# Optimization experiments

Hardware: AMD Instinct MI355X
Metric: run time of the kernel (lower is better)

The kernel has to match this reference:

```python
import jax, jax.numpy as jnp
import numpy as np

E = 65536          # number of edges (cell pairs)
D = 256            # hidden_dim
P = 8              # n_lr_pairs


def setup_inputs() -> dict:
    key = jax.random.key(0)
    k1, k2, k3, k4, k5, k6, k7 = jax.random.split(key, 7)
    scale = 1.0 / np.sqrt(D)
    z_src = jax.random.normal(k1, (E, D), dtype=jnp.float32)
    z_dst = jax.random.normal(k2, (E, D), dtype=jnp.float32)
    lr_pair_idx = jax.random.randint(k3, (E,), 0, P, dtype=jnp.int64)
    # Per-LR-pair Linear(D, D): y = x @ W.T + b  (torch convention, W: [out, in])
    W_lr = jax.random.normal(k4, (P, D, D), dtype=jnp.float32) * scale
    b_lr = jax.random.normal(k5, (P, D), dtype=jnp.float32) * scale
    # nn.Bilinear(D, D, 1): weight [1, D, D], bias [1]
    W_bil = jax.random.normal(k6, (1, D, D), dtype=jnp.float32) * scale
    b_bil = jax.random.normal(k7, (1,), dtype=jnp.float32) * scale
    return {"z_src": z_src, "z_dst": z_dst, "W_lr": W_lr, "b_lr": b_lr,
            "W_bil": W_bil, "b_bil": b_bil, "lr_pair_idx": lr_pair_idx}


def _forward(z_src, z_dst, W_lr, b_lr, W_bil, b_bil, lr_pair_idx):
    # Per-LR-pair linear projection of z_src (MoE-style routing).
    # Fixed small loop over P experts; each iteration is a dense GEMM over
    # all E edges, masked to the edges routed to that pair. All idx values
    # lie in [0, P), so the zeros-init in the original is fully overwritten.
    z_proj = jnp.zeros_like(z_src)
    for p in range(P):
        mask = (lr_pair_idx == p)[:, None]                      # [E, 1]
        y_p = z_src @ W_lr[p].T + b_lr[p]                       # [E, D]
        z_proj = jnp.where(mask, y_p, z_proj)
    # Bilinear scoring: score_e = z_proj_e @ W_bil[0] @ z_dst_e + b_bil
    t = z_proj @ W_bil[0]                                       # [E, D]
    scores = jnp.sum(t * z_dst, axis=-1, keepdims=True) + b_bil  # [E, 1]
    return scores


def reference(z_src, z_dst, W_lr, b_lr, W_bil, b_bil, lr_pair_idx):
    return _forward(z_src, z_dst, W_lr, b_lr, W_bil, b_bil, lr_pair_idx)
```

## Files before the change

### kernel.cpp

```cpp
#include <hip/hip_runtime.h>
#include <hip/hip_bf16.h>
#include <cstddef>

#define NE 65536
#define ND 256
#define NP 8
#define CAP 16384
#define TMAX 256
#define RBLK 64
#define EPB (NE / RBLK)

typedef short bf16x8 __attribute__((ext_vector_type(8)));
typedef float f32x4  __attribute__((ext_vector_type(4)));

__device__ __forceinline__ unsigned short f2bf(float f) {
  unsigned int u = __float_as_uint(f);
  u += 0x7FFFu + ((u >> 16) & 1u);
  return (unsigned short)(u >> 16);
}

__device__ __forceinline__ int sniff_is32(const void* idxraw, int* lflag) {
  int tid = threadIdx.x;
  if (tid == 0) *lflag = 0;
  __syncthreads();
  const unsigned int* w = (const unsigned int*)idxraw;
  unsigned int val = w[(blockIdx.x * 256 + tid) * 2 + 1];
  if (__any(val != 0) && (tid & 63) == 0) atomicOr(lflag, 1);
  __syncthreads();
  return *lflag;
}

__device__ __forceinline__ int load_idx(const void* idxraw, int is32, int e) {
  return is32 ? ((const int*)idxraw)[e] : (int)((const long long*)idxraw)[e];
}

__global__ __launch_bounds__(256) void k_hist(const void* __restrict__ idxraw,
                                              int* __restrict__ counts) {
  __shared__ int h[NP];
  __shared__ int lflag;
  int tid = threadIdx.x;
  int is32 = sniff_is32(idxraw, &lflag);
  if (tid < NP) h[tid] = 0;
  __syncthreads();
  int base = blockIdx.x * EPB;
#pragma unroll
  for (int i = 0; i < EPB / 256; ++i) {
    int p = load_idx(idxraw, is32, base + tid + i * 256);
    atomicAdd(&h[p], 1);
  }
  __syncthreads();
  if (tid < NP) counts[blockIdx.x * NP + tid] = h[tid];
}

__global__ __launch_bounds__(64) void k_scan(const int* __restrict__ counts,
                                             int* __restrict__ bases,
                                             int* __restrict__ cursor) {
  int q = threadIdx.x;
  if (q < NP) {
    int run = 0;
    for (int b = 0; b < RBLK; ++b) {
      bases[b * NP + q] = run;
      run += counts[b * NP + q];
    }
    cursor[q] = run;
  }
}

__global__ __launch_bounds__(256) void k_scatter(const void* __restrict__ idxraw,
                                                 const int* __restrict__ bases,
                                                 int* __restrict__ perm) {
  __shared__ int cur[NP];
  __shared__ int lflag;
  int tid = threadIdx.x;
  int is32 = sniff_is32(idxraw, &lflag);
  if (tid < NP) cur[tid] = bases[blockIdx.x * NP + tid];
  __syncthreads();
  int base = blockIdx.x * EPB;
#pragma unroll
  for (int i = 0; i < EPB / 256; ++i) {
    int e = base + tid + i * 256;
    int p = load_idx(idxraw, is32, e);
    int slot = atomicAdd(&cur[p], 1);
    perm[p * CAP + slot] = e;
  }
}

__global__ __launch_bounds__(256) void k_prep(const float* __restrict__ Wbil,
                                              const float* __restrict__ blr,
                                              unsigned short* __restrict__ WbT,
                                              float* __restrict__ v) {
  int b = blockIdx.x, t = threadIdx.x;
  if (b < 32) {
    int s = b * 256 + t;
    int kt = s >> 10, c = (s >> 6) & 15, l = s & 63;
    int col = c * 16 + (l & 15);
    int k0 = kt * 32 + (l >> 4) * 8;
    union { uint4 u; unsigned short h[8]; } uu;
#pragma unroll
    for (int j = 0; j < 8; ++j)
      uu.h[j] = f2bf(Wbil[(k0 + j) * ND + col]);
    *(uint4*)(WbT + (size_t)s * 8) = uu.u;
  } else {
    int p = b - 32;
    float s = 0.f;
    for (int k = 0; k < ND; ++k)
      s = fmaf(blr[p * ND + k], Wbil[k * ND + t], s);
    v[p * ND + t] = s;
  }
}

__global__ __launch_bounds__(256) void k_cpre(const float* __restrict__ Wlr,
                                              const unsigned short* __restrict__ WbT,
                                              unsigned short* __restrict__ Cst) {
  __shared__ unsigned short aF[2048 * 8];
  int blk = blockIdx.x;
  int p = blk >> 2;
  int i0 = (blk & 3) * 64;
  int tid = threadIdx.x;
  const float* Wp = Wlr + (size_t)p * ND * ND;
#pragma unroll
  for (int it = 0; it < 8; ++it) {
    int s = tid + it * 256;
    int kt = s >> 8, r = (s >> 6) & 3, l = s & 63;
    int i = r * 16 + (l & 15);
    int k0 = kt * 32 + (l >> 4) * 8;
    union { uint4 u; unsigned short h[8]; } uu;
#pragma unroll
    for (int j = 0; j < 8; ++j)
      uu.h[j] = f2bf(Wp[(size_t)(k0 + j) * ND + i0 + i]);
    *(uint4*)(aF + (size_t)s * 8) = uu.u;
  }
  __syncthreads();
  int w = tid >> 6, l = tid & 63;
  f32x4 zero = {0.f, 0.f, 0.f, 0.f};
  f32x4 acc[16];
#pragma unroll
  for (int c = 0; c < 16; ++c) acc[c] = zero;
  for (int kt = 0; kt < 8; ++kt) {
    bf16x8 a = *(const bf16x8*)(aF + (size_t)((kt * 4 + w) * 64 + l) * 8);
#pragma unroll
    for (int c = 0; c < 16; ++c) {
      bf16x8 bb = *(const bf16x8*)(WbT + (size_t)((kt * 16 + c) * 64 + l) * 8);
      acc[c] = __builtin_amdgcn_mfma_f32_16x16x32_bf16(a, bb, acc[c], 0, 0, 0);
    }
  }
  unsigned short* Cp = Cst + (size_t)p * ND * ND;
#pragma unroll
  for (int c = 0; c < 16; ++c) {
#pragma unroll
    for (int q = 0; q < 4; ++q) {
      int i = i0 + w * 16 + ((l >> 4) * 4) + q;
      int j = c * 16 + (l & 15);
      int pos = ((i >> 5) * 16 + (j >> 4)) * 512 + (((i >> 3) & 3) * 16 + (j & 15)) * 8 + (i & 7);
      Cp[pos] = f2bf(acc[c][q]);
    }
  }
}

__global__ __launch_bounds__(256, 2) void k_main(const float* __restrict__ zsrc,
                                                 const float* __restrict__ zdst,
                                                 const int* __restrict__ perm,
                                                 const int* __restrict__ cursor,
                                                 const unsigned short* __restrict__ Cst,
                                                 const float* __restrict__ v,
                                                 const float* __restrict__ bbil,
                                                 float* __restrict__ out) {
  int p = blockIdx.x >> 8;
  int t = blockIdx.x & 255;
  int cnt = cursor[p];
  if (t * 64 >= cnt) return;
  __shared__ unsigned short aF[2048 * 8];
  __shared__ unsigned short zL[64 * 256];
  __shared__ int eids[64];
  __shared__ float red[4][64];
  int tid = threadIdx.x;
  if (tid < 64) {
    int r = t * 64 + tid;
    eids[tid] = perm[p * CAP + (r < cnt ? r : cnt - 1)];
  }
  __syncthreads();
#pragma unroll
  for (int it = 0; it < 8; ++it) {
    int s = tid + it * 256;
    int kt = s >> 8, rr = (s >> 6) & 3, l = s & 63;
    int row = rr * 16 + (l & 15);
    int k0 = kt * 32 + (l >> 4) * 8;
    const float* src = zsrc + (size_t)eids[row] * ND + k0;
    const float* dsr = zdst + (size_t)eids[row] * ND + k0;
    float f[8], g[8];
    *(float4*)(f)     = *(const float4*)(src);
    *(float4*)(f + 4) = *(const float4*)(src + 4);
    *(float4*)(g)     = *(const float4*)(dsr);
    *(float4*)(g + 4) = *(const float4*)(dsr + 4);
    union { uint4 u; unsigned short h[8]; } ua, ud;
#pragma unroll
    for (int j = 0; j < 8; ++j) { ua.h[j] = f2bf(f[j]); ud.h[j] = f2bf(g[j]); }
    *(uint4*)(aF + (size_t)s * 8) = ua.u;
    unsigned int zb = (unsigned int)(row * 512 + k0 * 2) ^ (unsigned int)((row & 7) << 4);
    *(uint4*)((char*)zL + zb) = ud.u;
  }
  __syncthreads();
  int w = tid >> 6, l = tid & 63;
  const unsigned short* Cp = Cst + (size_t)p * ND * ND;
  f32x4 zero = {0.f, 0.f, 0.f, 0.f};
  f32x4 acc[4][4];
#pragma unroll
  for (int r = 0; r < 4; ++r)
#pragma unroll
    for (int c = 0; c < 4; ++c) acc[r][c] = zero;
  for (int kt = 0; kt < 8; ++kt) {
    bf16x8 a[4];
#pragma unroll
    for (int r = 0; r < 4; ++r)
      a[r] = *(const bf16x8*)(aF + (size_t)((kt * 4 + r) * 64 + l) * 8);
#pragma unroll
    for (int cl = 0; cl < 4; ++cl) {
      int c = w * 4 + cl;
      bf16x8 bb = *(const bf16x8*)(Cp + (size_t)((kt * 16 + c) * 64 + l) * 8);
#pragma unroll
      for (int r = 0; r < 4; ++r)
        acc[r][cl] = __builtin_amdgcn_mfma_f32_16x16x32_bf16(a[r], bb, acc[r][cl], 0, 0, 0);
    }
  }
  float vloc[4];
#pragma unroll
  for (int cl = 0; cl < 4; ++cl)
    vloc[cl] = v[p * ND + (w * 4 + cl) * 16 + (l & 15)];
#pragma unroll
  for (int r = 0; r < 4; ++r) {
#pragma unroll
    for (int q = 0; q < 4; ++q) {
      int row = r * 16 + ((l >> 4) * 4) + q;
      unsigned int swz = (unsigned int)((row & 7) << 4);
      float sv = 0.f;
#pragma unroll
      for (int cl = 0; cl < 4; ++cl) {
        int col = (w * 4 + cl) * 16 + (l & 15);
        unsigned int zb = (unsigned int)(row * 512 + col * 2) ^ swz;
        unsigned short hz = *(const unsigned short*)((const char*)zL + zb);
        float zv = __uint_as_float(((unsigned int)hz) << 16);
        sv = fmaf(acc[r][cl][q] + vloc[cl], zv, sv);
      }
      sv += __shfl_xor(sv, 1, 64);
      sv += __shfl_xor(sv, 2, 64);
      sv += __shfl_xor(sv, 4, 64);
      sv += __shfl_xor(sv, 8, 64);
      if ((l & 15) == 0) red[w][row] = sv;
    }
  }
  __syncthreads();
  if (tid < 64) {
    int gr = t * 64 + tid;
    if (gr < cnt) {
      float sc = red[0][tid] + red[1][tid] + red[2][tid] + red[3][tid] + bbil[0];
      out[eids[tid]] = sc;
    }
  }
}

extern "C" void kernel_launch(void* const* d_in, const int* in_sizes, int n_in,
                              void* d_out, int out_size, void* d_ws, size_t ws_size,
                              hipStream_t stream) {
  const float* zsrc = (const float*)d_in[0];
  const float* zdst = (const float*)d_in[1];
  const float* Wlr  = (const float*)d_in[2];
  const float* blr  = (const float*)d_in[3];
  const float* Wbil = (const float*)d_in[4];
  const float* bbil = (const float*)d_in[5];
  const void*  idx  = (const void*)d_in[6];
  float* out = (float*)d_out;

  char* ws = (char*)d_ws;
  int* cursor = (int*)ws;
  int* counts = (int*)(ws + 4096);
  int* bases  = (int*)(ws + 8192);
  int* perm   = (int*)(ws + 16384);
  unsigned short* WbT = (unsigned short*)(ws + 16384 + (size_t)NP * CAP * 4);
  float* v = (float*)(ws + 16384 + (size_t)NP * CAP * 4 + 131072);
  unsigned short* Cst = (unsigned short*)(ws + 16384 + (size_t)NP * CAP * 4 + 131072 + 8192);

  k_prep<<<40, 256, 0, stream>>>(Wbil, blr, WbT, v);
  k_hist<<<RBLK, 256, 0, stream>>>(idx, counts);
  k_scan<<<1, 64, 0, stream>>>(counts, bases, cursor);
  k_scatter<<<RBLK, 256, 0, stream>>>(idx, bases, perm);
  k_cpre<<<32, 256, 0, stream>>>(Wlr, WbT, Cst);
  k_main<<<NP * TMAX, 256, 0, stream>>>(zsrc, zdst, perm, cursor, Cst, v, bbil, out);
}
```

Baseline: 89.92 us.

## Compact per-pair permutation and coalesce row gathers in main kernel

Replaces the fixed-capacity per-pair permutation buckets with a compact global prefix-offset layout plus a tile-count header. This lets k_main launch only about as many blocks as there are real 64-row tiles, instead of 2048 blocks where most exit early. The gather of z_src and z_dst rows now has each wavefront read whole contiguous rows (one float4 per lane) rather than scattered 32-byte pieces, with the A-fragment layout remapped to match. The XOR swizzle on the z_dst LDS tile is dropped, which may bring back bank conflicts, and each block now pays a short linear search to find its pair.

```diff
diff --git a/kernel.cpp b/kernel.cpp
--- a/kernel.cpp
+++ b/kernel.cpp
@@ -5,8 +5,6 @@
 #define NE 65536
 #define ND 256
 #define NP 8
-#define CAP 16384
-#define TMAX 256
 #define RBLK 64
 #define EPB (NE / RBLK)
 
@@ -53,16 +51,37 @@
 }
 
 __global__ __launch_bounds__(64) void k_scan(const int* __restrict__ counts,
-                                             int* __restrict__ bases,
-                                             int* __restrict__ cursor) {
+                                             int* __restrict__ hdr,
+                                             int* __restrict__ bases) {
+  __shared__ int cnt[NP];
+  __shared__ int off[NP + 1];
   int q = threadIdx.x;
   if (q < NP) {
-    int run = 0;
+    int s = 0;
+    for (int b = 0; b < RBLK; ++b) s += counts[b * NP + q];
+    cnt[q] = s;
+  }
+  __syncthreads();
+  if (q == 0) {
+    int o = 0, tt = 0;
+    for (int p = 0; p < NP; ++p) {
+      off[p] = o;
+      hdr[p] = o;
+      hdr[9 + p] = tt;
+      o += cnt[p];
+      tt += (cnt[p] + 63) >> 6;
+    }
+    off[NP] = o;
+    hdr[NP] = o;
+    hdr[9 + NP] = tt;
+  }
+  __syncthreads();
+  if (q < NP) {
+    int run = off[q];
     for (int b = 0; b < RBLK; ++b) {
       bases[b * NP + q] = run;
       run += counts[b * NP + q];
     }
-    cursor[q] = run;
   }
 }
 
@@ -81,7 +100,7 @@
     int e = base + tid + i * 256;
     int p = load_idx(idxraw, is32, e);
     int slot = atomicAdd(&cur[p], 1);
-    perm[p * CAP + slot] = e;
+    perm[slot] = e;
   }
 }
 
@@ -160,47 +179,48 @@
 __global__ __launch_bounds__(256, 2) void k_main(const float* __restrict__ zsrc,
                                                  const float* __restrict__ zdst,
                                                  const int* __restrict__ perm,
-                                                 const int* __restrict__ cursor,
+                                                 const int* __restrict__ hdr,
                                                  const unsigned short* __restrict__ Cst,
                                                  const float* __restrict__ v,
                                                  const float* __restrict__ bbil,
                                                  float* __restrict__ out) {
-  int p = blockIdx.x >> 8;
-  int t = blockIdx.x & 255;
-  int cnt = cursor[p];
-  if (t * 64 >= cnt) return;
   __shared__ unsigned short aF[2048 * 8];
   __shared__ unsigned short zL[64 * 256];
   __shared__ int eids[64];
+  __shared__ int shdr[18];
   __shared__ float red[4][64];
   int tid = threadIdx.x;
+  if (tid < 18) shdr[tid] = hdr[tid];
+  __syncthreads();
+  int bid = blockIdx.x;
+  if (bid >= shdr[9 + NP]) return;
+  int p = 0;
+  while (p < NP - 1 && bid >= shdr[9 + p + 1]) ++p;
+  int t = bid - shdr[9 + p];
+  int cnt = shdr[p + 1] - shdr[p];
+  int ebase = shdr[p] + t * 64;
+  int nrow = cnt - t * 64; if (nrow > 64) nrow = 64;
   if (tid < 64) {
-    int r = t * 64 + tid;
-    eids[tid] = perm[p * CAP + (r < cnt ? r : cnt - 1)];
-  }
-  __syncthreads();
-#pragma unroll
-  for (int it = 0; it < 8; ++it) {
-    int s = tid + it * 256;
-    int kt = s >> 8, rr = (s >> 6) & 3, l = s & 63;
-    int row = rr * 16 + (l & 15);
-    int k0 = kt * 32 + (l >> 4) * 8;
-    const float* src = zsrc + (size_t)eids[row] * ND + k0;
-    const float* dsr = zdst + (size_t)eids[row] * ND + k0;
-    float f[8], g[8];
-    *(float4*)(f)     = *(const float4*)(src);
-    *(float4*)(f + 4) = *(const float4*)(src + 4);
-    *(float4*)(g)     = *(const float4*)(dsr);
-    *(float4*)(g + 4) = *(const float4*)(dsr + 4);
-    union { uint4 u; unsigned short h[8]; } ua, ud;
-#pragma unroll
-    for (int j = 0; j < 8; ++j) { ua.h[j] = f2bf(f[j]); ud.h[j] = f2bf(g[j]); }
-    *(uint4*)(aF + (size_t)s * 8) = ua.u;
-    unsigned int zb = (unsigned int)(row * 512 + k0 * 2) ^ (unsigned int)((row & 7) << 4);
-    *(uint4*)((char*)zL + zb) = ud.u;
+    int r = tid < nrow ? tid : nrow - 1;
+    eids[tid] = perm[ebase + r];
   }
   __syncthreads();
   int w = tid >> 6, l = tid & 63;
+#pragma unroll
+  for (int i = 0; i < 16; ++i) {
+    int row = w * 16 + i;
+    int e = eids[row];
+    f32x4 fs = ((const f32x4*)(zsrc + (size_t)e * ND))[l];
+    f32x4 fd = ((const f32x4*)(zdst + (size_t)e * ND))[l];
+    union { ushort4 u; unsigned short h[4]; } us, ud;
+#pragma unroll
+    for (int j = 0; j < 4; ++j) { us.h[j] = f2bf(fs[j]); ud.h[j] = f2bf(fd[j]); }
+    *(ushort4*)((char*)zL + row * 512 + l * 8) = ud.u;
+    int slot = ((l >> 3) * 4 + w) * 64 + ((l & 7) >> 1) * 16 + i;
+    *(ushort4*)((char*)aF + slot * 16 + (l & 1) * 8) = us.u;
+  }
+  __syncthreads();
+
   const unsigned short* Cp = Cst + (size_t)p * ND * ND;
   f32x4 zero = {0.f, 0.f, 0.f, 0.f};
   f32x4 acc[4][4];
@@ -208,6 +228,7 @@
   for (int r = 0; r < 4; ++r)
 #pragma unroll
     for (int c = 0; c < 4; ++c) acc[r][c] = zero;
+#pragma unroll
   for (int kt = 0; kt < 8; ++kt) {
     bf16x8 a[4];
 #pragma unroll
@@ -215,8 +236,7 @@
       a[r] = *(const bf16x8*)(aF + (size_t)((kt * 4 + r) * 64 + l) * 8);
 #pragma unroll
     for (int cl = 0; cl < 4; ++cl) {
-      int c = w * 4 + cl;
-      bf16x8 bb = *(const bf16x8*)(Cp + (size_t)((kt * 16 + c) * 64 + l) * 8);
+      bf16x8 bb = *(const bf16x8*)(Cp + (size_t)((kt * 16 + w * 4 + cl) * 64 + l) * 8);
 #pragma unroll
       for (int r = 0; r < 4; ++r)
         acc[r][cl] = __builtin_amdgcn_mfma_f32_16x16x32_bf16(a[r], bb, acc[r][cl], 0, 0, 0);
@@ -231,13 +251,11 @@
 #pragma unroll
     for (int q = 0; q < 4; ++q) {
       int row = r * 16 + ((l >> 4) * 4) + q;
-      unsigned int swz = (unsigned int)((row & 7) << 4);
       float sv = 0.f;
 #pragma unroll
       for (int cl = 0; cl < 4; ++cl) {
         int col = (w * 4 + cl) * 16 + (l & 15);
-        unsigned int zb = (unsigned int)(row * 512 + col * 2) ^ swz;
-        unsigned short hz = *(const unsigned short*)((const char*)zL + zb);
+        unsigned short hz = zL[row * 256 + col];
         float zv = __uint_as_float(((unsigned int)hz) << 16);
         sv = fmaf(acc[r][cl][q] + vloc[cl], zv, sv);
       }
@@ -249,12 +267,9 @@
     }
   }
   __syncthreads();
-  if (tid < 64) {
-    int gr = t * 64 + tid;
-    if (gr < cnt) {
-      float sc = red[0][tid] + red[1][tid] + red[2][tid] + red[3][tid] + bbil[0];
-      out[eids[tid]] = sc;
-    }
+  if (tid < 64 && tid < nrow) {
+    float sc = red[0][tid] + red[1][tid] + red[2][tid] + red[3][tid] + bbil[0];
+    out[eids[tid]] = sc;
   }
 }
 
@@ -271,18 +286,18 @@
   float* out = (float*)d_out;
 
   char* ws = (char*)d_ws;
-  int* cursor = (int*)ws;
+  int* hdr    = (int*)ws;
   int* counts = (int*)(ws + 4096);
   int* bases  = (int*)(ws + 8192);
   int* perm   = (int*)(ws + 16384);
-  unsigned short* WbT = (unsigned short*)(ws + 16384 + (size_t)NP * CAP * 4);
-  float* v = (float*)(ws + 16384 + (size_t)NP * CAP * 4 + 131072);
-  unsigned short* Cst = (unsigned short*)(ws + 16384 + (size_t)NP * CAP * 4 + 131072 + 8192);
+  unsigned short* WbT = (unsigned short*)(ws + 16384 + (size_t)NE * 4);
+  float* v = (float*)(ws + 16384 + (size_t)NE * 4 + 131072);
+  unsigned short* Cst = (unsigned short*)(ws + 16384 + (size_t)NE * 4 + 131072 + 8192);
 
   k_prep<<<40, 256, 0, stream>>>(Wbil, blr, WbT, v);
   k_hist<<<RBLK, 256, 0, stream>>>(idx, counts);
-  k_scan<<<1, 64, 0, stream>>>(counts, bases, cursor);
+  k_scan<<<1, 64, 0, stream>>>(counts, hdr, bases);
   k_scatter<<<RBLK, 256, 0, stream>>>(idx, bases, perm);
   k_cpre<<<32, 256, 0, stream>>>(Wlr, WbT, Cst);
-  k_main<<<NP * TMAX, 256, 0, stream>>>(zsrc, zdst, perm, cursor, Cst, v, bbil, out);
-}
+  k_main<<<1032, 256, 0, stream>>>(zsrc, zdst, perm, hdr, Cst, v, bbil, out);
+}
```

Measured after the change: 88.96 us. No clear change (-1.1%).
